# Performance work log

Measured on AMD Instinct MI355X. Metric: run time of the kernel, lower is better.

Reference implementation:

```python
import jax, jax.numpy as jnp
import numpy as np


def setup_inputs() -> dict:
    key = jax.random.key(0)
    ks = jax.random.split(key, 7)
    B, N, D = 8, 2048, 512
    s = 1.0 / np.sqrt(D)
    return {
        "x": jax.random.normal(ks[0], (B, N, D), dtype=jnp.float32),
        "Wq": jax.random.normal(ks[1], (D, D), dtype=jnp.float32) * s,
        "bq": jax.random.normal(ks[2], (D,), dtype=jnp.float32) * 0.01,
        "Wk": jax.random.normal(ks[3], (D, D), dtype=jnp.float32) * s,
        "bk": jax.random.normal(ks[4], (D,), dtype=jnp.float32) * 0.01,
        "Wv": jax.random.normal(ks[5], (D, D), dtype=jnp.float32) * s,
        "bv": jax.random.normal(ks[6], (D,), dtype=jnp.float32) * 0.01,
    }


def reference(x, Wq, bq, Wk, bk, Wv, bv):
    # Linear layers: x @ W.T + b (torch nn.Linear convention, weight [out,in])
    q = jnp.einsum("bnd,ed->bne", x, Wq) + bq
    k = jnp.einsum("bnd,ed->bne", x, Wk) + bk
    v = jnp.einsum("bnd,ed->bne", x, Wv) + bv
    # Unscaled attention scores, softmax over keys
    att = jax.nn.softmax(jnp.einsum("bne,bme->bnm", q, k), axis=-1)  # [B,N,N]
    # Original's broadcast-multiply+sum over dim=1 == att @ v
    return jnp.einsum("bnm,bme->bne", att, v)  # [B,N,D]
```

## Files before the change

kernel.cpp:

```cpp
#include <hip/hip_runtime.h>

typedef __attribute__((ext_vector_type(8))) _Float16 f16x8;
typedef __attribute__((ext_vector_type(8))) unsigned short u16x8;
typedef __attribute__((ext_vector_type(4))) float f32x4;
typedef unsigned short u16;

__device__ __forceinline__ u16 f2h(float f) {
  _Float16 h = (_Float16)f;
  return __builtin_bit_cast(u16, h);
}
__device__ __forceinline__ float h2f(u16 u) {
  return (float)__builtin_bit_cast(_Float16, u);
}

__device__ __forceinline__ void gl_lds16(const u16* g, u16* l) {
  __builtin_amdgcn_global_load_lds(
      (const __attribute__((address_space(1))) void*)g,
      (__attribute__((address_space(3))) void*)l, 16, 0, 0);
}

__global__ __launch_bounds__(256) void cvt_h(const float* __restrict__ in,
                                             u16* __restrict__ hi, int n8) {
  int t = blockIdx.x * 256 + threadIdx.x;
  if (t >= n8) return;
  const float4* p = (const float4*)in;
  float4 a = p[2 * t], b = p[2 * t + 1];
  float v[8] = {a.x, a.y, a.z, a.w, b.x, b.y, b.z, b.w};
  u16x8 h;
#pragma unroll
  for (int i = 0; i < 8; ++i) h[i] = f2h(v[i]);
  *(u16x8*)(hi + (size_t)t * 8) = h;
}

__device__ __forceinline__ void mfma_core1(u16* s, const u16* __restrict__ A,
                                           const u16* __restrict__ B,
                                           int lda, int ldb, int Kdim,
                                           int m0, int n0, f32x4 acc[4][4]) {
  const int tid = threadIdx.x;
  const int l = tid & 63, w = tid >> 6;
  const int wm = w >> 1, wn = w & 1;
  const int quad = l >> 4, l15 = l & 15;
  const int srow = w * 32 + (l >> 2);
  const int skc = (l & 3) * 8;

  u16* sA = s;
  u16* sB = s + 4096;

  const u16* gA0 = A + (size_t)(m0 + srow) * lda + skc;
  const u16* gB0 = B + (size_t)(n0 + srow) * ldb + skc;
  u16* lA0 = sA + srow * 32 + skc;
  u16* lB0 = sB + srow * 32 + skc;
  const size_t a16 = (size_t)16 * lda, b16 = (size_t)16 * ldb;

  const int afrag = (wm * 64 + l15) * 32 + quad * 8;
  const int bfrag = (wn * 64 + l15) * 32 + quad * 8;

  for (int k0 = 0; k0 < Kdim; k0 += 32) {
    __syncthreads();
    gl_lds16(gA0 + k0, lA0);
    gl_lds16(gA0 + k0 + a16, lA0 + 512);
    gl_lds16(gB0 + k0, lB0);
    gl_lds16(gB0 + k0 + b16, lB0 + 512);
    __syncthreads();

    f16x8 fa[4], fb[4];
#pragma unroll
    for (int i = 0; i < 4; ++i) fa[i] = *(const f16x8*)(sA + afrag + i * 512);
#pragma unroll
    for (int j = 0; j < 4; ++j) fb[j] = *(const f16x8*)(sB + bfrag + j * 512);
#pragma unroll
    for (int i = 0; i < 4; ++i)
#pragma unroll
      for (int j = 0; j < 4; ++j)
        acc[i][j] = __builtin_amdgcn_mfma_f32_16x16x32_f16(fa[i], fb[j],
                                                           acc[i][j], 0, 0, 0);
  }
}

__global__ __launch_bounds__(256, 2) void gemm_f32o(
    const u16* __restrict__ A, const u16* __restrict__ B, float* __restrict__ C,
    int lda, int ldb, int ldc, int Kdim, size_t aStride, size_t bStride,
    size_t cStride) {
  __shared__ u16 s[8192];
  const int z = blockIdx.z;
  f32x4 acc[4][4];
  const f32x4 zero = {0.0f, 0.0f, 0.0f, 0.0f};
#pragma unroll
  for (int i = 0; i < 4; ++i)
#pragma unroll
    for (int j = 0; j < 4; ++j) acc[i][j] = zero;
  mfma_core1(s, A + z * aStride, B + z * bStride, lda, ldb, Kdim,
             blockIdx.y * 128, blockIdx.x * 128, acc);
  float* Cz = C + z * cStride;
  const int lane = threadIdx.x & 63;
  const int wave = threadIdx.x >> 6;
  const int quad = lane >> 4, l15 = lane & 15;
  const int em = (int)blockIdx.y * 128 + (wave >> 1) * 64 + quad * 4;
  const int en = (int)blockIdx.x * 128 + (wave & 1) * 64 + l15;
#pragma unroll
  for (int i = 0; i < 4; ++i)
#pragma unroll
    for (int r = 0; r < 4; ++r) {
      size_t row = (size_t)(em + i * 16 + r) * ldc;
#pragma unroll
      for (int j = 0; j < 4; ++j) Cz[row + en + j * 16] = acc[i][j][r];
    }
}

__global__ __launch_bounds__(256, 2) void gemm_qkv4(
    const u16* __restrict__ xh, const u16* __restrict__ Wq,
    const u16* __restrict__ Wk, const u16* __restrict__ Wv,
    const float* __restrict__ bq, const float* __restrict__ bk,
    const float* __restrict__ bv, u16* __restrict__ Q, u16* __restrict__ K,
    u16* __restrict__ Vt, int ldvt) {
  __shared__ u16 s[8192];
  const int z = blockIdx.x >> 2;
  const int n0 = (blockIdx.x & 3) * 128;
  const int m0 = blockIdx.y * 128;
  const u16* W = (z == 0) ? Wq : (z == 1) ? Wk : Wv;
  const float* bias = (z == 0) ? bq : (z == 1) ? bk : bv;
  f32x4 acc[4][4];
  const f32x4 zero = {0.0f, 0.0f, 0.0f, 0.0f};
#pragma unroll
  for (int i = 0; i < 4; ++i)
#pragma unroll
    for (int j = 0; j < 4; ++j) acc[i][j] = zero;

  mfma_core1(s, xh, W, 512, 512, 512, m0, n0, acc);

  const int lane = threadIdx.x & 63;
  const int wave = threadIdx.x >> 6;
  const int quad = lane >> 4, l15 = lane & 15;
  const int em = m0 + (wave >> 1) * 64 + quad * 4;
  const int en = n0 + (wave & 1) * 64 + l15;
  float bj[4];
#pragma unroll
  for (int j = 0; j < 4; ++j) bj[j] = bias[en + j * 16];
  if (z < 2) {
    u16* O = (z == 0) ? Q : K;
#pragma unroll
    for (int i = 0; i < 4; ++i)
#pragma unroll
      for (int r = 0; r < 4; ++r) {
        size_t row = (size_t)(em + i * 16 + r) * 512;
#pragma unroll
        for (int j = 0; j < 4; ++j)
          O[row + en + j * 16] = f2h(acc[i][j][r] + bj[j]);
      }
  } else {
#pragma unroll
    for (int i = 0; i < 4; ++i)
#pragma unroll
      for (int r = 0; r < 4; ++r) {
        int m = em + i * 16 + r;
#pragma unroll
        for (int j = 0; j < 4; ++j)
          Vt[(size_t)(en + j * 16) * ldvt + m] = f2h(acc[i][j][r] + bj[j]);
      }
  }
}

__global__ __launch_bounds__(256) void softmax_inplace(float* __restrict__ S) {
  __shared__ float red[8];
  const int tid = threadIdx.x;
  const size_t row = blockIdx.x;
  const float4* src = (const float4*)(S + row * 2048);
  float4 v0 = src[2 * tid], v1 = src[2 * tid + 1];

  float mx = fmaxf(fmaxf(fmaxf(v0.x, v0.y), fmaxf(v0.z, v0.w)),
                   fmaxf(fmaxf(v1.x, v1.y), fmaxf(v1.z, v1.w)));
#pragma unroll
  for (int off = 32; off >= 1; off >>= 1) mx = fmaxf(mx, __shfl_xor(mx, off));
  const int wid = tid >> 6, lane = tid & 63;
  if (lane == 0) red[wid] = mx;
  __syncthreads();
  if (tid == 0) red[4] = fmaxf(fmaxf(red[0], red[1]), fmaxf(red[2], red[3]));
  __syncthreads();
  mx = red[4];

  v0.x = __expf(v0.x - mx); v0.y = __expf(v0.y - mx);
  v0.z = __expf(v0.z - mx); v0.w = __expf(v0.w - mx);
  v1.x = __expf(v1.x - mx); v1.y = __expf(v1.y - mx);
  v1.z = __expf(v1.z - mx); v1.w = __expf(v1.w - mx);

  float sm = v0.x + v0.y + v0.z + v0.w + v1.x + v1.y + v1.z + v1.w;
#pragma unroll
  for (int off = 32; off >= 1; off >>= 1) sm += __shfl_xor(sm, off);
  __syncthreads();
  if (lane == 0) red[wid] = sm;
  __syncthreads();
  if (tid == 0) red[5] = red[0] + red[1] + red[2] + red[3];
  __syncthreads();
  const float inv = 1.0f / red[5];

  u16x8 o;
  o[0] = f2h(v0.x * inv); o[1] = f2h(v0.y * inv);
  o[2] = f2h(v0.z * inv); o[3] = f2h(v0.w * inv);
  o[4] = f2h(v1.x * inv); o[5] = f2h(v1.y * inv);
  o[6] = f2h(v1.z * inv); o[7] = f2h(v1.w * inv);
  *(u16x8*)((u16*)S + row * 4096 + tid * 8) = o;
}

#define LTILE_M 64
#define LTILE_N 64
#define LTILE_K 32
template <bool B_NT, bool HAS_BIAS>
__device__ __forceinline__ void gemm_body_leg(const float* __restrict__ A,
                                              const float* __restrict__ Bm,
                                              const float* __restrict__ bias,
                                              float* __restrict__ C, int lda,
                                              int ldb, int ldc, int Kdim) {
  __shared__ float As[LTILE_K][LTILE_M + 4];
  __shared__ float Bs[LTILE_K][LTILE_N + 4];
  const int tid = threadIdx.x;
  const int tx = tid & 15, ty = tid >> 4;
  const int m0 = blockIdx.y * LTILE_M, n0 = blockIdx.x * LTILE_N;
  const int am = tid >> 3, ak = (tid & 7) << 2;
  const int bk_ = tid >> 4, bn = (tid & 15) << 2;
  float acc[4][4] = {};
  for (int k0 = 0; k0 < Kdim; k0 += LTILE_K) {
    float4 a0 = *(const float4*)(A + (size_t)(m0 + am) * lda + k0 + ak);
    float4 a1 = *(const float4*)(A + (size_t)(m0 + am + 32) * lda + k0 + ak);
    float4 b0, b1;
    if (B_NT) {
      b0 = *(const float4*)(Bm + (size_t)(n0 + am) * ldb + k0 + ak);
      b1 = *(const float4*)(Bm + (size_t)(n0 + am + 32) * ldb + k0 + ak);
    } else {
      b0 = *(const float4*)(Bm + (size_t)(k0 + bk_) * ldb + n0 + bn);
      b1 = *(const float4*)(Bm + (size_t)(k0 + bk_ + 16) * ldb + n0 + bn);
    }
    __syncthreads();
    As[ak + 0][am] = a0.x; As[ak + 1][am] = a0.y;
    As[ak + 2][am] = a0.z; As[ak + 3][am] = a0.w;
    As[ak + 0][am + 32] = a1.x; As[ak + 1][am + 32] = a1.y;
    As[ak + 2][am + 32] = a1.z; As[ak + 3][am + 32] = a1.w;
    if (B_NT) {
      Bs[ak + 0][am] = b0.x; Bs[ak + 1][am] = b0.y;
      Bs[ak + 2][am] = b0.z; Bs[ak + 3][am] = b0.w;
      Bs[ak + 0][am + 32] = b1.x; Bs[ak + 1][am + 32] = b1.y;
      Bs[ak + 2][am + 32] = b1.z; Bs[ak + 3][am + 32] = b1.w;
    } else {
      *(float4*)&Bs[bk_][bn] = b0;
      *(float4*)&Bs[bk_ + 16][bn] = b1;
    }
    __syncthreads();
#pragma unroll
    for (int kk = 0; kk < LTILE_K; ++kk) {
      float4 av = *(const float4*)&As[kk][ty << 2];
      float4 bv4 = *(const float4*)&Bs[kk][tx << 2];
      acc[0][0] += av.x * bv4.x; acc[0][1] += av.x * bv4.y;
      acc[0][2] += av.x * bv4.z; acc[0][3] += av.x * bv4.w;
      acc[1][0] += av.y * bv4.x; acc[1][1] += av.y * bv4.y;
      acc[1][2] += av.y * bv4.z; acc[1][3] += av.y * bv4.w;
      acc[2][0] += av.z * bv4.x; acc[2][1] += av.z * bv4.y;
      acc[2][2] += av.z * bv4.z; acc[2][3] += av.z * bv4.w;
      acc[3][0] += av.w * bv4.x; acc[3][1] += av.w * bv4.y;
      acc[3][2] += av.w * bv4.z; acc[3][3] += av.w * bv4.w;
    }
  }
  float4 badd = {0.0f, 0.0f, 0.0f, 0.0f};
  if (HAS_BIAS) badd = *(const float4*)(bias + n0 + (tx << 2));
#pragma unroll
  for (int r = 0; r < 4; ++r) {
    float4 o;
    o.x = acc[r][0] + badd.x; o.y = acc[r][1] + badd.y;
    o.z = acc[r][2] + badd.z; o.w = acc[r][3] + badd.w;
    *(float4*)(C + (size_t)(m0 + (ty << 2) + r) * ldc + n0 + (tx << 2)) = o;
  }
}
template <bool B_NT, bool HAS_BIAS>
__global__ __launch_bounds__(256, 4) void gemm_leg(const float* A, const float* Bm,
                                                   const float* bias, float* C,
                                                   int lda, int ldb, int ldc,
                                                   int Kdim) {
  gemm_body_leg<B_NT, HAS_BIAS>(A, Bm, bias, C, lda, ldb, ldc, Kdim);
}
__global__ __launch_bounds__(256, 4) void qkv_leg(
    const float* x, const float* Wq, const float* bq, const float* Wk,
    const float* bk, const float* Wv, const float* bv, float* Q, float* K,
    float* V) {
  const float *W, *bias;
  float* C;
  if (blockIdx.z == 0) { W = Wq; bias = bq; C = Q; }
  else if (blockIdx.z == 1) { W = Wk; bias = bk; C = K; }
  else { W = Wv; bias = bv; C = V; }
  gemm_body_leg<true, true>(x, W, bias, C, 512, 512, 512, 512);
}
__global__ __launch_bounds__(256) void softmax_leg(float* S, int ncols) {
  __shared__ float red[8];
  float4* rowp = (float4*)(S + (size_t)blockIdx.x * ncols);
  const int tid = threadIdx.x;
  float4 v0 = rowp[tid], v1 = rowp[tid + 256];
  float mx = fmaxf(fmaxf(fmaxf(v0.x, v0.y), fmaxf(v0.z, v0.w)),
                   fmaxf(fmaxf(v1.x, v1.y), fmaxf(v1.z, v1.w)));
#pragma unroll
  for (int off = 32; off >= 1; off >>= 1) mx = fmaxf(mx, __shfl_xor(mx, off));
  const int wid = tid >> 6, lane = tid & 63;
  if (lane == 0) red[wid] = mx;
  __syncthreads();
  if (tid == 0) red[4] = fmaxf(fmaxf(red[0], red[1]), fmaxf(red[2], red[3]));
  __syncthreads();
  mx = red[4];
  v0.x = __expf(v0.x - mx); v0.y = __expf(v0.y - mx);
  v0.z = __expf(v0.z - mx); v0.w = __expf(v0.w - mx);
  v1.x = __expf(v1.x - mx); v1.y = __expf(v1.y - mx);
  v1.w = __expf(v1.w - mx); v1.z = __expf(v1.z - mx);
  float sm = v0.x + v0.y + v0.z + v0.w + v1.x + v1.y + v1.z + v1.w;
#pragma unroll
  for (int off = 32; off >= 1; off >>= 1) sm += __shfl_xor(sm, off);
  __syncthreads();
  if (lane == 0) red[wid] = sm;
  __syncthreads();
  if (tid == 0) red[5] = red[0] + red[1] + red[2] + red[3];
  __syncthreads();
  const float inv = 1.0f / red[5];
  v0.x *= inv; v0.y *= inv; v0.z *= inv; v0.w *= inv;
  v1.x *= inv; v1.y *= inv; v1.z *= inv; v1.w *= inv;
  rowp[tid] = v0;
  rowp[tid + 256] = v1;
}

extern "C" void kernel_launch(void* const* d_in, const int* in_sizes, int n_in,
                              void* d_out, int out_size, void* d_ws,
                              size_t ws_size, hipStream_t stream) {
  (void)in_sizes; (void)n_in; (void)out_size;
  const int B = 8, N = 2048, D = 512;
  const size_t ND = (size_t)N * D;
  const size_t NN = (size_t)N * N;
  const float* x = (const float*)d_in[0];
  const float* Wf[3] = {(const float*)d_in[1], (const float*)d_in[3],
                        (const float*)d_in[5]};
  const float* bq = (const float*)d_in[2];
  const float* bk = (const float*)d_in[4];
  const float* bv = (const float*)d_in[6];
  float* out = (float*)d_out;

  char* w = (char*)d_ws;
  auto take = [&](size_t bytes) {
    char* p = w;
    w += (bytes + 255) & ~(size_t)255;
    return p;
  };

  if (ws_size >= 190000000ULL) {
    u16* Wh[3];
    for (int i = 0; i < 3; ++i) Wh[i] = (u16*)take(524288);
    u16* Q  = (u16*)take(2 * B * ND);
    u16* K  = (u16*)take(2 * B * ND);
    u16* Vt = (u16*)take(2 * B * ND);
    float* S = (float*)w;
    u16* xh = (u16*)take(2 * B * ND);

    cvt_h<<<8192, 256, 0, stream>>>(x, xh, (int)(B * ND / 8));
    for (int i = 0; i < 3; ++i)
      cvt_h<<<128, 256, 0, stream>>>(Wf[i], Wh[i], 32768);
    gemm_qkv4<<<dim3(12, 128), 256, 0, stream>>>(
        xh, Wh[0], Wh[1], Wh[2], bq, bk, bv, Q, K, Vt, B * N);
    gemm_f32o<<<dim3(16, 16, 8), 256, 0, stream>>>(
        Q, K, S, 512, 512, 2048, 512, ND, ND, NN);
    softmax_inplace<<<B * N, 256, 0, stream>>>(S);
    gemm_f32o<<<dim3(4, 16, 8), 256, 0, stream>>>(
        (const u16*)S, Vt, out, 4096, B * N, 512, 2048, 2 * NN, (size_t)N, ND);
  } else {
    float* ws = (float*)d_ws;
    float* Q = ws;
    float* Kp = ws + ND;
    float* V = ws + 2 * ND;
    float* S = ws + 3 * ND;
    for (int b = 0; b < B; ++b) {
      const float* xb = x + b * ND;
      float* outb = out + b * ND;
      qkv_leg<<<dim3(8, 32, 3), 256, 0, stream>>>(xb, Wf[0], bq, Wf[1], bk,
                                                  Wf[2], bv, Q, Kp, V);
      gemm_leg<true, false><<<dim3(32, 32), 256, 0, stream>>>(Q, Kp, nullptr, S,
                                                              512, 512, 2048, 512);
      softmax_leg<<<N, 256, 0, stream>>>(S, N);
      gemm_leg<false, false><<<dim3(8, 32), 256, 0, stream>>>(S, V, nullptr,
                                                              outb, 2048, 512,
                                                              512, 2048);
    }
  }
}
```

Measured before the change: 324.5 us.

## Split-K the PV GEMM with atomic accumulation and interleave batches across workgroups

The P·V GEMM is split four ways along the key dimension into 2048 workgroups that accumulate into a zeroed output with float atomicAdd, replacing the 512-workgroup launch. Both the scores and PV GEMMs now use a flat 1D grid with the batch index in the low bits, so neighbouring workgroups work on different batches. This is meant to fill the GPU better for the long-K PV GEMM, at the cost of a memset, atomic traffic and non-deterministic summation order. Shared epilogue code is factored into macros.

```diff
diff --git a/kernel.cpp b/kernel.cpp
--- a/kernel.cpp
+++ b/kernel.cpp
@@ -5,12 +5,12 @@
 typedef __attribute__((ext_vector_type(4))) float f32x4;
 typedef unsigned short u16;
 
+#define NDC 1048576UL
+#define NNC 4194304UL
+
 __device__ __forceinline__ u16 f2h(float f) {
   _Float16 h = (_Float16)f;
   return __builtin_bit_cast(u16, h);
-}
-__device__ __forceinline__ float h2f(u16 u) {
-  return (float)__builtin_bit_cast(_Float16, u);
 }
 
 __device__ __forceinline__ void gl_lds16(const u16* g, u16* l) {
@@ -77,35 +77,20 @@
   }
 }
 
-__global__ __launch_bounds__(256, 2) void gemm_f32o(
-    const u16* __restrict__ A, const u16* __restrict__ B, float* __restrict__ C,
-    int lda, int ldb, int ldc, int Kdim, size_t aStride, size_t bStride,
-    size_t cStride) {
-  __shared__ u16 s[8192];
-  const int z = blockIdx.z;
-  f32x4 acc[4][4];
-  const f32x4 zero = {0.0f, 0.0f, 0.0f, 0.0f};
-#pragma unroll
-  for (int i = 0; i < 4; ++i)
-#pragma unroll
-    for (int j = 0; j < 4; ++j) acc[i][j] = zero;
-  mfma_core1(s, A + z * aStride, B + z * bStride, lda, ldb, Kdim,
-             blockIdx.y * 128, blockIdx.x * 128, acc);
-  float* Cz = C + z * cStride;
-  const int lane = threadIdx.x & 63;
-  const int wave = threadIdx.x >> 6;
-  const int quad = lane >> 4, l15 = lane & 15;
-  const int em = (int)blockIdx.y * 128 + (wave >> 1) * 64 + quad * 4;
-  const int en = (int)blockIdx.x * 128 + (wave & 1) * 64 + l15;
-#pragma unroll
-  for (int i = 0; i < 4; ++i)
-#pragma unroll
-    for (int r = 0; r < 4; ++r) {
-      size_t row = (size_t)(em + i * 16 + r) * ldc;
-#pragma unroll
-      for (int j = 0; j < 4; ++j) Cz[row + en + j * 16] = acc[i][j][r];
-    }
-}
+#define ACC_ZERO()                                   \
+  f32x4 acc[4][4];                                   \
+  {                                                  \
+    const f32x4 zero = {0.0f, 0.0f, 0.0f, 0.0f};     \
+    for (int i = 0; i < 4; ++i)                      \
+      for (int j = 0; j < 4; ++j) acc[i][j] = zero;  \
+  }
+
+#define EPI_COORDS(mbase, nbase)                            \
+  const int lane = threadIdx.x & 63;                        \
+  const int wave = threadIdx.x >> 6;                        \
+  const int quad = lane >> 4, l15 = lane & 15;              \
+  const int em = (mbase) + (wave >> 1) * 64 + quad * 4;     \
+  const int en = (nbase) + (wave & 1) * 64 + l15;
 
 __global__ __launch_bounds__(256, 2) void gemm_qkv4(
     const u16* __restrict__ xh, const u16* __restrict__ Wq,
@@ -119,20 +104,9 @@
   const int m0 = blockIdx.y * 128;
   const u16* W = (z == 0) ? Wq : (z == 1) ? Wk : Wv;
   const float* bias = (z == 0) ? bq : (z == 1) ? bk : bv;
-  f32x4 acc[4][4];
-  const f32x4 zero = {0.0f, 0.0f, 0.0f, 0.0f};
-#pragma unroll
-  for (int i = 0; i < 4; ++i)
-#pragma unroll
-    for (int j = 0; j < 4; ++j) acc[i][j] = zero;
-
+  ACC_ZERO();
   mfma_core1(s, xh, W, 512, 512, 512, m0, n0, acc);
-
-  const int lane = threadIdx.x & 63;
-  const int wave = threadIdx.x >> 6;
-  const int quad = lane >> 4, l15 = lane & 15;
-  const int em = m0 + (wave >> 1) * 64 + quad * 4;
-  const int en = n0 + (wave & 1) * 64 + l15;
+  EPI_COORDS(m0, n0);
   float bj[4];
 #pragma unroll
   for (int j = 0; j < 4; ++j) bj[j] = bias[en + j * 16];
@@ -158,6 +132,56 @@
           Vt[(size_t)(en + j * 16) * ldvt + m] = f2h(acc[i][j][r] + bj[j]);
       }
   }
+}
+
+__global__ __launch_bounds__(256, 2) void gemm_scores(
+    const u16* __restrict__ Q, const u16* __restrict__ K,
+    float* __restrict__ S) {
+  __shared__ u16 s[8192];
+  const int wg = blockIdx.x;
+  const int z = wg & 7;
+  const int t = wg >> 3;
+  const int n0 = (t & 15) * 128;
+  const int m0 = (t >> 4) * 128;
+  ACC_ZERO();
+  mfma_core1(s, Q + z * NDC, K + z * NDC, 512, 512, 512, m0, n0, acc);
+  float* Sz = S + z * NNC;
+  EPI_COORDS(m0, n0);
+#pragma unroll
+  for (int i = 0; i < 4; ++i)
+#pragma unroll
+    for (int r = 0; r < 4; ++r) {
+      size_t row = (size_t)(em + i * 16 + r) * 2048;
+#pragma unroll
+      for (int j = 0; j < 4; ++j) Sz[row + en + j * 16] = acc[i][j][r];
+    }
+}
+
+__global__ __launch_bounds__(256, 2) void gemm_pv(
+    const u16* __restrict__ P, const u16* __restrict__ Vt,
+    float* __restrict__ out) {
+  __shared__ u16 s[8192];
+  const int wg = blockIdx.x;
+  const int z = wg & 7;
+  const int t = wg >> 3;
+  const int n0 = (t & 3) * 128;
+  const int kc = (t >> 2) & 3;
+  const int m0 = (t >> 4) * 128;
+  const u16* Pz = P + z * 2 * NNC + kc * 512;
+  const u16* Vz = Vt + z * 2048 + kc * 512;
+  ACC_ZERO();
+  mfma_core1(s, Pz, Vz, 4096, 16384, 512, m0, n0, acc);
+  float* oz = out + z * NDC;
+  EPI_COORDS(m0, n0);
+#pragma unroll
+  for (int i = 0; i < 4; ++i)
+#pragma unroll
+    for (int r = 0; r < 4; ++r) {
+      size_t row = (size_t)(em + i * 16 + r) * 512;
+#pragma unroll
+      for (int j = 0; j < 4; ++j)
+        atomicAdd(&oz[row + en + j * 16], acc[i][j][r]);
+    }
 }
 
 __global__ __launch_bounds__(256) void softmax_inplace(float* __restrict__ S) {
@@ -323,7 +347,7 @@
 extern "C" void kernel_launch(void* const* d_in, const int* in_sizes, int n_in,
                               void* d_out, int out_size, void* d_ws,
                               size_t ws_size, hipStream_t stream) {
-  (void)in_sizes; (void)n_in; (void)out_size;
+  (void)in_sizes; (void)n_in;
   const int B = 8, N = 2048, D = 512;
   const size_t ND = (size_t)N * D;
   const size_t NN = (size_t)N * N;
@@ -356,11 +380,10 @@
       cvt_h<<<128, 256, 0, stream>>>(Wf[i], Wh[i], 32768);
     gemm_qkv4<<<dim3(12, 128), 256, 0, stream>>>(
         xh, Wh[0], Wh[1], Wh[2], bq, bk, bv, Q, K, Vt, B * N);
-    gemm_f32o<<<dim3(16, 16, 8), 256, 0, stream>>>(
-        Q, K, S, 512, 512, 2048, 512, ND, ND, NN);
+    gemm_scores<<<2048, 256, 0, stream>>>(Q, K, S);
     softmax_inplace<<<B * N, 256, 0, stream>>>(S);
-    gemm_f32o<<<dim3(4, 16, 8), 256, 0, stream>>>(
-        (const u16*)S, Vt, out, 4096, B * N, 512, 2048, 2 * NN, (size_t)N, ND);
+    hipMemsetAsync(out, 0, (size_t)out_size * sizeof(float), stream);
+    gemm_pv<<<2048, 256, 0, stream>>>((const u16*)S, Vt, out);
   } else {
     float* ws = (float*)d_ws;
     float* Q = ws;
```

New measurement: 367.4 us. +13.2%, slower.
